# Performance work log

Hardware: AMD Instinct MI355X
Metric: run time of the kernel (lower is better)

## Reference

```python
import jax, jax.numpy as jnp
import numpy as np
import math

C, B, T, D = 8, 4, 4096, 128
MAX_LEN = 8192


def _lambdas():
    # geometrically spaced fixed decays: lam_c = 1 - 2^{-c*delta}
    delta = math.log2(MAX_LEN) / max(C - 1, 1)
    return jnp.array([1.0 - 2.0 ** (-(c * delta)) for c in range(C)], dtype=jnp.float32)


def _fixed_decay_scan(lam, v):
    """h_t = lam_c * h_{t-1} + v_t along axis 2. lam: (C,), v: (C,B,T,D).
    Uses an associative scan (log-depth), equivalent to the doubling trick.
    lam=0 channels reduce to identity automatically."""
    a = jnp.broadcast_to(lam[:, None, None, None], (v.shape[0], 1, v.shape[2], 1))

    def combine(x, y):
        a1, b1 = x
        a2, b2 = y
        return (a1 * a2, a2 * b1 + b2)

    _, h = jax.lax.associative_scan(combine, (a, v), axis=2)
    return h


def _run_direction(z, W, b, lam):
    # per-channel learned input gate: g = sigmoid(z @ W_c + b_c)
    g = jax.nn.sigmoid(jnp.einsum('cbtd,cde->cbte', z, W) + b[:, None, None, :])
    return _fixed_decay_scan(lam, g * z)


def setup_inputs() -> dict:
    key = jax.random.key(0)
    k1, k2, k3, k4, k5 = jax.random.split(key, 5)
    return {
        'channels': jax.random.normal(k1, (C, B, T, D), dtype=jnp.float32),
        'Wf': jax.random.normal(k2, (C, D, D), dtype=jnp.float32) * 0.02,
        'bf': jax.random.normal(k3, (C, D), dtype=jnp.float32),
        'Wb': jax.random.normal(k4, (C, D, D), dtype=jnp.float32) * 0.02,
        'bb': jax.random.normal(k5, (C, D), dtype=jnp.float32),
    }


def reference(channels, Wf, bf, Wb, bb):
    lam = _lambdas()
    fwd = _run_direction(channels, Wf, bf, lam)
    # backward direction: flip time, scan, flip back
    rev = channels[:, :, ::-1, :]
    bwd = _run_direction(rev, Wb, bb, lam)[:, :, ::-1, :]
    return (fwd, bwd)
```

## Files before the change

### kernel.cpp

```cpp
#include <hip/hip_runtime.h>
#include <hip/hip_bf16.h>
#include <math.h>

#define C_ 8
#define B_ 4
#define T_ 4096
#define D_ 128
#define TT 64
#define NCH (T_ / TT)
#define CBTD ((size_t)C_ * B_ * T_ * D_)
#define SSIZE ((size_t)2 * C_ * B_ * NCH * D_)
#define LOG2E 1.44269504088896f

typedef __attribute__((ext_vector_type(8))) short short8;
typedef __attribute__((ext_vector_type(4))) float f32x4;
typedef __attribute__((ext_vector_type(8))) unsigned short u16x8;
typedef __attribute__((ext_vector_type(4))) unsigned short u16x4;

__device__ __forceinline__ float lam_of(int c) {
  return (float)(1.0 - exp2(-(double)c * (13.0 / 7.0)));
}

__device__ __forceinline__ float decay_pow(float lam, float l2lam, int n) {
  if (n == 0) return 1.0f;
  if (lam == 0.0f) return 0.0f;
  return exp2f((float)n * l2lam);
}

__device__ __forceinline__ unsigned short f2bf(float x) {
  __hip_bfloat16 h = __float2bfloat16(x);
  unsigned short u;
  __builtin_memcpy(&u, &h, 2);
  return u;
}

__global__ __launch_bounds__(256)
void wcvt_kernel(const float* __restrict__ Wf, const float* __restrict__ Wb,
                 unsigned short* __restrict__ Wt) {
  __shared__ unsigned short Tq[128][130];
  const int blk = blockIdx.x;
  const float* src = ((blk & 8) ? Wb : Wf) + (size_t)(blk & 7) * D_ * D_;
  const int tid = threadIdx.x;
  for (int i = 0; i < 16; ++i) {
    int fidx = tid + 256 * i;
    int d = fidx >> 5, e4 = (fidx & 31) * 4;
    float4 v = *(const float4*)(src + (size_t)d * D_ + e4);
    Tq[e4 + 0][d] = f2bf(v.x * LOG2E);
    Tq[e4 + 1][d] = f2bf(v.y * LOG2E);
    Tq[e4 + 2][d] = f2bf(v.z * LOG2E);
    Tq[e4 + 3][d] = f2bf(v.w * LOG2E);
  }
  __syncthreads();
  short8* dst = (short8*)(Wt + (size_t)blk * D_ * D_);
  for (int i = 0; i < 8; ++i) {
    int o = tid + 256 * i;
    int f = o >> 8, ks = (o >> 6) & 3, l4s = (o >> 4) & 3, l15s = o & 15;
    short8 t;
    #pragma unroll
    for (int j = 0; j < 8; ++j)
      t[j] = (short)Tq[f * 16 + l15s][ks * 32 + l4s * 8 + j];
    dst[o] = t;
  }
}

__global__ __launch_bounds__(256)
void gate_mfma_kernel(const float* __restrict__ z,
                      const unsigned short* __restrict__ Wt,
                      const float* __restrict__ bf, const float* __restrict__ bb,
                      float* __restrict__ out, float* __restrict__ S) {
  __shared__ float term[2][16][132];
  __shared__ unsigned short sb16[64][136];

  const int bi = blockIdx.x;
  const int tile = bi & (NCH - 1);
  const int b = (bi >> 6) & (B_ - 1);
  const int c = bi >> 8;
  const int tid = threadIdx.x;
  const int lane = tid & 63;
  const int w = tid >> 6;
  const int l15 = lane & 15;
  const int l4 = lane >> 4;

  const float lam = lam_of(c);
  float lp[5];
  lp[0] = 1.f;
  #pragma unroll
  for (int i = 1; i < 5; ++i) lp[i] = lp[i - 1] * lam;

  const float* zsrc = z + ((size_t)(c * B_ + b) * T_ + tile * TT) * D_;

  short8 afrag[4];
  const int rowA = w * 16 + l15;
  #pragma unroll
  for (int ks = 0; ks < 4; ++ks) {
    const float* p = zsrc + (size_t)rowA * D_ + ks * 32 + l4 * 8;
    float4 a0 = *(const float4*)p;
    float4 a1 = *(const float4*)(p + 4);
    short8 t;
    t[0] = (short)f2bf(a0.x); t[1] = (short)f2bf(a0.y);
    t[2] = (short)f2bf(a0.z); t[3] = (short)f2bf(a0.w);
    t[4] = (short)f2bf(a1.x); t[5] = (short)f2bf(a1.y);
    t[6] = (short)f2bf(a1.z); t[7] = (short)f2bf(a1.w);
    afrag[ks] = t;
  }

  float zreg[8][4];
  const int rowE = w * 16 + l4 * 4;
  #pragma unroll
  for (int f = 0; f < 8; ++f)
    #pragma unroll
    for (int r = 0; r < 4; ++r)
      zreg[f][r] = zsrc[(size_t)(rowE + r) * D_ + f * 16 + l15];

  const short8* wf0 = (const short8*)(Wt + (size_t)(0 * 8 + c) * D_ * D_);
  const short8* wf1 = (const short8*)(Wt + (size_t)(1 * 8 + c) * D_ * D_);

  f32x4 acc[2][8];
  #pragma unroll
  for (int d = 0; d < 2; ++d)
    #pragma unroll
    for (int f = 0; f < 8; ++f) acc[d][f] = (f32x4){0.f, 0.f, 0.f, 0.f};

  #pragma unroll
  for (int f = 0; f < 8; ++f) {
    #pragma unroll
    for (int ks = 0; ks < 4; ++ks) {
      short8 b0 = wf0[(f * 4 + ks) * 64 + lane];
      short8 b1 = wf1[(f * 4 + ks) * 64 + lane];
      acc[0][f] = __builtin_amdgcn_mfma_f32_16x16x32_bf16(afrag[ks], b0, acc[0][f], 0, 0, 0);
      acc[1][f] = __builtin_amdgcn_mfma_f32_16x16x32_bf16(afrag[ks], b1, acc[1][f], 0, 0, 0);
    }
  }

  #pragma unroll
  for (int d = 0; d < 2; ++d) {
    const float* bias = (d ? bb : bf) + (size_t)c * D_;
    #pragma unroll
    for (int f = 0; f < 8; ++f) {
      const float bcol = bias[f * 16 + l15] * LOG2E;
      float vv[4];
      #pragma unroll
      for (int r = 0; r < 4; ++r) {
        const float logit = acc[d][f][r] + bcol;
        const float g = __builtin_amdgcn_rcpf(1.0f + exp2f(-logit));
        vv[r] = g * zreg[f][r];
      }
      if (d == 0) {
        float h = 0.f;
        #pragma unroll
        for (int r = 0; r < 4; ++r) { h = fmaf(lam, h, vv[r]); acc[d][f][r] = h; }
      } else {
        float h = 0.f;
        #pragma unroll
        for (int r = 3; r >= 0; --r) { h = fmaf(lam, h, vv[r]); acc[d][f][r] = h; }
      }
      term[d][w * 4 + l4][f * 16 + l15] = (d == 0) ? acc[d][f][3] : acc[d][f][0];
    }
  }
  __syncthreads();

  {
    const int d = tid >> 7;
    const int col = tid & 127;
    float tg[16];
    #pragma unroll
    for (int g = 0; g < 16; ++g) tg[g] = term[d][g][col];
    float p = 0.f;
    const float l4p = lp[4];
    if (d == 0) {
      #pragma unroll
      for (int g = 0; g < 16; ++g) { float t = tg[g]; term[d][g][col] = p; p = fmaf(l4p, p, t); }
    } else {
      #pragma unroll
      for (int g = 15; g >= 0; --g) { float t = tg[g]; term[d][g][col] = p; p = fmaf(l4p, p, t); }
    }
    S[(((size_t)(d * C_ + c) * B_ + b) * NCH + tile) * D_ + col] = p;
  }

  #pragma unroll
  for (int d = 0; d < 2; ++d) {
    __syncthreads();
    #pragma unroll
    for (int f = 0; f < 8; ++f) {
      const int col = f * 16 + l15;
      const float carry = term[d][w * 4 + l4][col];
      #pragma unroll
      for (int r = 0; r < 4; ++r) {
        const float dec = (d == 0) ? lp[r + 1] : lp[4 - r];
        sb16[rowE + r][col] = f2bf(fmaf(dec, carry, acc[d][f][r]));
      }
    }
    __syncthreads();
    float* dst = out + (size_t)d * CBTD +
                 ((size_t)(c * B_ + b) * T_ + tile * TT) * D_;
    if (c == 0) {
      #pragma unroll
      for (int i = 0; i < 8; ++i) {
        int fidx = tid + 256 * i;
        int row = fidx >> 5, col4 = (fidx & 31) * 4;
        u16x4 hv = *(const u16x4*)&sb16[row][col4];
        f32x4 v;
        v.x = __uint_as_float((unsigned)hv[0] << 16);
        v.y = __uint_as_float((unsigned)hv[1] << 16);
        v.z = __uint_as_float((unsigned)hv[2] << 16);
        v.w = __uint_as_float((unsigned)hv[3] << 16);
        __builtin_nontemporal_store(v, (f32x4*)(dst + (size_t)row * D_ + col4));
      }
    } else {
      unsigned short* hb = (unsigned short*)dst;
      #pragma unroll
      for (int i = 0; i < 4; ++i) {
        int fidx = tid + 256 * i;
        int row = fidx >> 4, c8 = (fidx & 15) * 8;
        u16x8 o = *(const u16x8*)&sb16[row][c8];
        __builtin_nontemporal_store(o, (u16x8*)(hb + row * 128 + c8));
      }
    }
  }
}

__global__ __launch_bounds__(128)
void prefix_kernel(const float* __restrict__ S, float* __restrict__ Cin) {
  const int bi = blockIdx.x;
  const int dir = bi >> 5;
  const int c = (bi >> 2) & 7;
  const int b = bi & 3;
  const int e = threadIdx.x;
  const float lam = lam_of(c);
  const float l2lam = (lam > 0.f) ? log2f(lam) : 0.f;
  const float lamL = decay_pow(lam, l2lam, TT);
  const size_t base = ((size_t)(dir * C_ + c) * B_ + b) * NCH * D_ + e;
  float cin = 0.f;
  if (dir == 0) {
    for (int k = 0; k < NCH; ++k) {
      Cin[base + (size_t)k * D_] = cin;
      cin = fmaf(lamL, cin, S[base + (size_t)k * D_]);
    }
  } else {
    for (int k = NCH - 1; k >= 0; --k) {
      Cin[base + (size_t)k * D_] = cin;
      cin = fmaf(lamL, cin, S[base + (size_t)k * D_]);
    }
  }
}

__global__ __launch_bounds__(256)
void apply_kernel(float* __restrict__ out, const float* __restrict__ Cin) {
  const int bi = blockIdx.x;
  const int k = bi & (NCH - 1);
  const int b = (bi >> 6) & 3;
  const int c = (bi >> 8) & 7;
  const int dir = bi >> 11;
  if (c == 0) return;
  const float lam = lam_of(c);
  const float l2lam = log2f(lam);
  const int tid = threadIdx.x;
  const int col4 = (tid & 31) * 4;

  const f32x4 carry = *(const f32x4*)
      (Cin + (((size_t)(dir * C_ + c) * B_ + b) * NCH + k) * D_ + col4);
  float* base = out + (size_t)dir * CBTD +
                ((size_t)(c * B_ + b) * T_ + k * TT) * D_;
  const unsigned short* hb = (const unsigned short*)base;

  u16x4 hv[8];
  #pragma unroll
  for (int i = 0; i < 8; ++i) {
    const int row = (tid >> 5) + i * 8;
    hv[i] = *(const u16x4*)(hb + row * 128 + col4);
  }
  __syncthreads();

  #pragma unroll
  for (int i = 0; i < 8; ++i) {
    const int row = (tid >> 5) + i * 8;
    const int dist = (dir == 0) ? (row + 1) : (TT - row);
    const float dec = exp2f(l2lam * (float)dist);
    f32x4 h;
    h.x = fmaf(dec, carry.x, __uint_as_float((unsigned)hv[i][0] << 16));
    h.y = fmaf(dec, carry.y, __uint_as_float((unsigned)hv[i][1] << 16));
    h.z = fmaf(dec, carry.z, __uint_as_float((unsigned)hv[i][2] << 16));
    h.w = fmaf(dec, carry.w, __uint_as_float((unsigned)hv[i][3] << 16));
    __builtin_nontemporal_store(h, (f32x4*)(base + (size_t)row * D_ + col4));
  }
}

extern "C" void kernel_launch(void* const* d_in, const int* in_sizes, int n_in,
                              void* d_out, int out_size, void* d_ws, size_t ws_size,
                              hipStream_t stream) {
  const float* z  = (const float*)d_in[0];
  const float* Wf = (const float*)d_in[1];
  const float* bf = (const float*)d_in[2];
  const float* Wb = (const float*)d_in[3];
  const float* bb = (const float*)d_in[4];
  float* out = (float*)d_out;
  float* S   = (float*)d_ws;
  float* Cin = S + SSIZE;
  unsigned short* Wt = (unsigned short*)(Cin + SSIZE);

  wcvt_kernel<<<dim3(16), dim3(256), 0, stream>>>(Wf, Wb, Wt);
  gate_mfma_kernel<<<dim3(C_ * B_ * NCH), dim3(256), 0, stream>>>(
      z, Wt, bf, bb, out, S);
  prefix_kernel<<<dim3(2 * C_ * B_), dim3(128), 0, stream>>>(S, Cin);
  apply_kernel<<<dim3(2 * C_ * B_ * NCH), dim3(256), 0, stream>>>(out, Cin);
}
```

Measured before the change: 79.38 us.

## Store bf16 intermediates in MFMA fragment order, skipping LDS staging

For channels c>0, the gate kernel now writes its bf16 intra-tile results straight from registers in the MFMA accumulator fragment order. This removes the LDS round-trip and two barriers per direction. The apply kernel reads that permuted layout with 16-byte loads, adds the carry term, and re-transposes through a shared-memory buffer to write row-major fp32 output. The cost moves into the apply kernel, which now uses LDS staging and extra barriers; the intermediate layout must match exactly between the two kernels.

```diff
diff --git a/kernel.cpp b/kernel.cpp
--- a/kernel.cpp
+++ b/kernel.cpp
@@ -176,24 +176,25 @@
     }
     S[(((size_t)(d * C_ + c) * B_ + b) * NCH + tile) * D_ + col] = p;
   }
-
-  #pragma unroll
-  for (int d = 0; d < 2; ++d) {
-    __syncthreads();
-    #pragma unroll
-    for (int f = 0; f < 8; ++f) {
-      const int col = f * 16 + l15;
-      const float carry = term[d][w * 4 + l4][col];
-      #pragma unroll
-      for (int r = 0; r < 4; ++r) {
-        const float dec = (d == 0) ? lp[r + 1] : lp[4 - r];
-        sb16[rowE + r][col] = f2bf(fmaf(dec, carry, acc[d][f][r]));
-      }
-    }
-    __syncthreads();
-    float* dst = out + (size_t)d * CBTD +
-                 ((size_t)(c * B_ + b) * T_ + tile * TT) * D_;
-    if (c == 0) {
+  __syncthreads();
+
+  if (c == 0) {
+    #pragma unroll
+    for (int d = 0; d < 2; ++d) {
+      if (d) __syncthreads();
+      #pragma unroll
+      for (int f = 0; f < 8; ++f) {
+        const int col = f * 16 + l15;
+        const float carry = term[d][w * 4 + l4][col];
+        #pragma unroll
+        for (int r = 0; r < 4; ++r) {
+          const float dec = (d == 0) ? lp[r + 1] : lp[4 - r];
+          sb16[rowE + r][col] = f2bf(fmaf(dec, carry, acc[d][f][r]));
+        }
+      }
+      __syncthreads();
+      float* dst = out + (size_t)d * CBTD +
+                   ((size_t)(c * B_ + b) * T_ + tile * TT) * D_;
       #pragma unroll
       for (int i = 0; i < 8; ++i) {
         int fidx = tid + 256 * i;
@@ -206,14 +207,24 @@
         v.w = __uint_as_float((unsigned)hv[3] << 16);
         __builtin_nontemporal_store(v, (f32x4*)(dst + (size_t)row * D_ + col4));
       }
-    } else {
-      unsigned short* hb = (unsigned short*)dst;
-      #pragma unroll
-      for (int i = 0; i < 4; ++i) {
-        int fidx = tid + 256 * i;
-        int row = fidx >> 4, c8 = (fidx & 15) * 8;
-        u16x8 o = *(const u16x8*)&sb16[row][c8];
-        __builtin_nontemporal_store(o, (u16x8*)(hb + row * 128 + c8));
+    }
+  } else {
+    #pragma unroll
+    for (int d = 0; d < 2; ++d) {
+      unsigned short* hb = (unsigned short*)(out + (size_t)d * CBTD +
+                           ((size_t)(c * B_ + b) * T_ + tile * TT) * D_);
+      #pragma unroll
+      for (int slot = 0; slot < 4; ++slot) {
+        u16x8 o;
+        #pragma unroll
+        for (int e = 0; e < 8; ++e) {
+          const int f = slot * 2 + (e >> 2);
+          const int r = e & 3;
+          const float dec = (d == 0) ? lp[r + 1] : lp[4 - r];
+          const float carry = term[d][w * 4 + l4][f * 16 + l15];
+          o[e] = f2bf(fmaf(dec, carry, acc[d][f][r]));
+        }
+        __builtin_nontemporal_store(o, (u16x8*)(hb + ((size_t)slot * 256 + tid) * 8));
       }
     }
   }
@@ -246,6 +257,9 @@
 
 __global__ __launch_bounds__(256)
 void apply_kernel(float* __restrict__ out, const float* __restrict__ Cin) {
+  __shared__ float sbuf[64][132];
+  __shared__ float gcar[128];
+
   const int bi = blockIdx.x;
   const int k = bi & (NCH - 1);
   const int b = (bi >> 6) & 3;
@@ -255,33 +269,48 @@
   const float lam = lam_of(c);
   const float l2lam = log2f(lam);
   const int tid = threadIdx.x;
-  const int col4 = (tid & 31) * 4;
-
-  const f32x4 carry = *(const f32x4*)
-      (Cin + (((size_t)(dir * C_ + c) * B_ + b) * NCH + k) * D_ + col4);
+
+  if (tid < 128)
+    gcar[tid] = Cin[(((size_t)(dir * C_ + c) * B_ + b) * NCH + k) * D_ + tid];
+
   float* base = out + (size_t)dir * CBTD +
                 ((size_t)(c * B_ + b) * T_ + k * TT) * D_;
   const unsigned short* hb = (const unsigned short*)base;
 
-  u16x4 hv[8];
+  const int roww = ((tid >> 6) << 4) + (((tid >> 4) & 3) << 2);
+  const int l15 = tid & 15;
+  float dec[4];
+  #pragma unroll
+  for (int r = 0; r < 4; ++r) {
+    const int dist = (dir == 0) ? (roww + r + 1) : (TT - (roww + r));
+    dec[r] = exp2f(l2lam * (float)dist);
+  }
+
+  u16x8 hv[4];
+  #pragma unroll
+  for (int slot = 0; slot < 4; ++slot)
+    hv[slot] = *(const u16x8*)(hb + ((size_t)slot * 256 + tid) * 8);
+  __syncthreads();
+
+  #pragma unroll
+  for (int slot = 0; slot < 4; ++slot) {
+    #pragma unroll
+    for (int e = 0; e < 8; ++e) {
+      const int f = slot * 2 + (e >> 2);
+      const int r = e & 3;
+      const int col = f * 16 + l15;
+      const float v = __uint_as_float((unsigned)(unsigned short)hv[slot][e] << 16);
+      sbuf[roww + r][col] = fmaf(dec[r], gcar[col], v);
+    }
+  }
+  __syncthreads();
+
   #pragma unroll
   for (int i = 0; i < 8; ++i) {
-    const int row = (tid >> 5) + i * 8;
-    hv[i] = *(const u16x4*)(hb + row * 128 + col4);
-  }
-  __syncthreads();
-
-  #pragma unroll
-  for (int i = 0; i < 8; ++i) {
-    const int row = (tid >> 5) + i * 8;
-    const int dist = (dir == 0) ? (row + 1) : (TT - row);
-    const float dec = exp2f(l2lam * (float)dist);
-    f32x4 h;
-    h.x = fmaf(dec, carry.x, __uint_as_float((unsigned)hv[i][0] << 16));
-    h.y = fmaf(dec, carry.y, __uint_as_float((unsigned)hv[i][1] << 16));
-    h.z = fmaf(dec, carry.z, __uint_as_float((unsigned)hv[i][2] << 16));
-    h.w = fmaf(dec, carry.w, __uint_as_float((unsigned)hv[i][3] << 16));
-    __builtin_nontemporal_store(h, (f32x4*)(base + (size_t)row * D_ + col4));
+    int fidx = tid + 256 * i;
+    int row = fidx >> 5, col4 = (fidx & 31) * 4;
+    f32x4 v = *(const f32x4*)&sbuf[row][col4];
+    __builtin_nontemporal_store(v, (f32x4*)(base + (size_t)row * D_ + col4));
   }
 }
 
```

Measured after the change: 85.50 us. 1.08x slower.
